# Kernel optimization log

Measured on AMD Instinct MI355X. Metric: run time of the kernel, lower is better.

## Reference

```python
import jax, jax.numpy as jnp
import numpy as np

B, S, D, H, DFF = 4, 1024, 1024, 16, 4096
DK = D // H
EPS = 1e-6


def setup_inputs() -> dict:
    key = jax.random.key(0)
    ks = jax.random.split(key, 16)
    sd = 0.02
    inp = {
        "x_v": jax.random.normal(ks[0], (B, S, D), jnp.float32),
        "x_k": jax.random.normal(ks[1], (B, S, D), jnp.float32),
        "x_q": jax.random.normal(ks[2], (B, S, D), jnp.float32),
        "mask": jnp.zeros((B, 1, S), jnp.float32),
        # per-head projections stacked: [H, D, DK]
        "wq": jax.random.normal(ks[3], (H, D, DK), jnp.float32) * sd,
        "bq": jnp.zeros((H, DK), jnp.float32),
        "wk": jax.random.normal(ks[4], (H, D, DK), jnp.float32) * sd,
        "bk": jnp.zeros((H, DK), jnp.float32),
        "wv": jax.random.normal(ks[5], (H, D, DK), jnp.float32) * sd,
        "bv": jnp.zeros((H, DK), jnp.float32),
        "w0": jax.random.normal(ks[6], (D, D), jnp.float32) * sd,
        "b0": jnp.zeros((D,), jnp.float32),
        "ln1_g": jnp.ones((D,), jnp.float32),
        "ln1_b": jnp.zeros((D,), jnp.float32),
        "ff1_w": jax.random.normal(ks[7], (D, DFF), jnp.float32) * sd,
        "ff1_b": jnp.zeros((DFF,), jnp.float32),
        "ff2_w": jax.random.normal(ks[8], (DFF, D), jnp.float32) * sd,
        "ff2_b": jnp.zeros((D,), jnp.float32),
        "ln2_g": jnp.ones((D,), jnp.float32),
        "ln2_b": jnp.zeros((D,), jnp.float32),
    }
    return inp


def layer_norm(x, g, b):
    mu = jnp.mean(x, axis=-1, keepdims=True)
    var = jnp.mean(jnp.square(x - mu), axis=-1, keepdims=True)
    return (x - mu) * jax.lax.rsqrt(var + EPS) * g + b


def reference(x_v, x_k, x_q, mask, wq, bq, wk, bk, wv, bv, w0, b0,
              ln1_g, ln1_b, ff1_w, ff1_b, ff2_w, ff2_b, ln2_g, ln2_b):
    # --- Multi-head attention (heads batched instead of Python loop) ---
    q = jnp.einsum('bsd,hdk->bhsk', x_q, wq) + bq[:, None, :]  # [B,H,S,DK]
    k = jnp.einsum('bsd,hdk->bhsk', x_k, wk) + bk[:, None, :]
    v = jnp.einsum('bsd,hdk->bhsk', x_v, wv) + bv[:, None, :]
    scores = jnp.einsum('bhqk,bhsk->bhqs', q, k) / jnp.sqrt(jnp.float32(DK))
    scores = scores + mask[:, None, :, :] * (-1e9)  # mask broadcast over heads
    attn_w = jax.nn.softmax(scores, axis=-1)        # [B,H,S,S]
    attn = jnp.einsum('bhqs,bhsk->bhqk', attn_w, v)  # [B,H,S,DK]
    concat = attn.transpose(0, 2, 1, 3).reshape(B, S, D)
    mha_out = concat @ w0 + b0
    # --- Residual + LayerNorm 1 (dropout is identity at inference) ---
    sub1 = layer_norm(x_q + mha_out, ln1_g, ln1_b)
    # --- Point-wise FFN ---
    ffn = jax.nn.relu(sub1 @ ff1_w + ff1_b) @ ff2_w + ff2_b
    # --- Residual + LayerNorm 2 ---
    out = layer_norm(sub1 + ffn, ln2_g, ln2_b)
    # original returns the attention weights of the LAST head only
    return out, attn_w[:, -1]
```

## Files before the change

### kernel.cpp

```cpp
#include <hip/hip_runtime.h>
#include <hip/hip_bf16.h>
#include <stdint.h>

#define DEV __device__ __forceinline__

typedef uint16_t u16;
typedef __attribute__((ext_vector_type(8))) short s16x8;
typedef __attribute__((ext_vector_type(8))) unsigned short u16x8;
typedef __attribute__((ext_vector_type(4))) unsigned short u16x4;
typedef __attribute__((ext_vector_type(4))) float f32x4;

constexpr int CB = 4;
constexpr int CS = 1024;
constexpr int CD = 1024;
constexpr int CH = 16;
constexpr int CDFF = 4096;
constexpr int KVB = 128;
constexpr int LSTRP = 136;
constexpr float QSCALE = 0.125f * 1.44269504f;
constexpr float MASKC  = -1.44269504e9f;

DEV float b2f(u16 u) { union { uint32_t i; float f; } v; v.i = (uint32_t)u << 16; return v.f; }
DEV u16 f2b(float f) {
  union { float f; uint32_t i; } v; v.f = f;
  uint32_t r = v.i + 0x7fffu + ((v.i >> 16) & 1u);
  return (u16)(r >> 16);
}
DEV float ex2(float x) {
#if __has_builtin(__builtin_amdgcn_exp2f)
  return __builtin_amdgcn_exp2f(x);
#else
  return __expf(x * 0.69314718056f);
#endif
}

using as1v = const __attribute__((address_space(1))) void;
using as3v = __attribute__((address_space(3))) void;
DEV void g2l16(const u16* g, u16* l) {
  __builtin_amdgcn_global_load_lds((as1v*)g, (as3v*)l, 16, 0, 0);
}

__global__ void detect_dtype(const uint32_t* __restrict__ w, uint32_t* __restrict__ flag) {
  if (threadIdx.x == 0 && blockIdx.x == 0) {
    flag[0] = (w[0] == 0x3F800000u) ? 1u : 0u;
    flag[1] = 0u;
  }
}

__global__ __launch_bounds__(256)
void cvt3(const void* __restrict__ s0, const void* __restrict__ s1, const void* __restrict__ s2,
          u16* __restrict__ d0, u16* __restrict__ d1, u16* __restrict__ d2,
          const uint32_t* __restrict__ flag)
{
  const void* s = blockIdx.z == 0 ? s0 : (blockIdx.z == 1 ? s1 : s2);
  u16* d        = blockIdx.z == 0 ? d0 : (blockIdx.z == 1 ? d1 : d2);
  size_t i = ((size_t)blockIdx.x * 256 + threadIdx.x) * 4;
  if (flag[0]) {
    const float* f = (const float*)s;
    u16x4 o;
#pragma unroll
    for (int j = 0; j < 4; j++) o[j] = f2b(f[i + j]);
    *(u16x4*)(d + i) = o;
  } else {
    *(u16x4*)(d + i) = *(const u16x4*)((const u16*)s + i);
  }
}

struct SmallCvt {
  const void* src[11];
  u16* dst[11];
  int n[11];
};
__global__ __launch_bounds__(256)
void cvt_small(SmallCvt sc, const uint32_t* __restrict__ flag)
{
  int idx = blockIdx.x * 256 + threadIdx.x;
#pragma unroll
  for (int a = 0; a < 11; a++) {
    if (idx < sc.n[a]) {
      if (flag[0]) sc.dst[a][idx] = f2b(((const float*)sc.src[a])[idx]);
      else         sc.dst[a][idx] = ((const u16*)sc.src[a])[idx];
      return;
    }
    idx -= sc.n[a];
  }
}

__global__ __launch_bounds__(256)
void transpose64d(const void* __restrict__ in, u16* __restrict__ out,
                  int in_rs, long long in_ys, long long in_zs,
                  int out_rs, long long out_ys, long long out_zs,
                  const uint32_t* __restrict__ flag)
{
  int t = blockIdx.x * 256 + threadIdx.x;
  int k  = t & 63;
  int n8 = t >> 6;
  size_t ib = (size_t)blockIdx.z * in_zs + (size_t)blockIdx.y * in_ys
            + (size_t)n8 * 8 * in_rs + k;
  u16* ob = out + (size_t)blockIdx.z * out_zs + (size_t)blockIdx.y * out_ys
                + (size_t)k * out_rs + (size_t)n8 * 8;
  u16x8 v;
  if (flag[0]) {
    const float* f = (const float*)in;
#pragma unroll
    for (int j = 0; j < 8; j++) v[j] = f2b(f[ib + (size_t)j * in_rs]);
  } else {
    const u16* u = (const u16*)in;
#pragma unroll
    for (int j = 0; j < 8; j++) v[j] = u[ib + (size_t)j * in_rs];
  }
  *(u16x8*)ob = v;
}

struct TBatch {
  const void* in[6];
  u16* out[6];
  int in_rs[6];
  long long in_ys[6];
  int out_rs[6];
  long long out_ys[6];
  int nx[6];
  int cnt[6];
};
__global__ __launch_bounds__(256)
void transpose_batch(TBatch tb, const uint32_t* __restrict__ flag)
{
  int rem = blockIdx.x;
  int e = 0;
  while (e < 5 && rem >= tb.cnt[e]) { rem -= tb.cnt[e]; e++; }
  const int bx = rem % tb.nx[e];
  const int by = rem / tb.nx[e];
  const int in_rs = tb.in_rs[e];
  int t = bx * 256 + threadIdx.x;
  int k  = t & 63;
  int n8 = t >> 6;
  size_t ib = (size_t)by * tb.in_ys[e] + (size_t)n8 * 8 * in_rs + k;
  u16* ob = tb.out[e] + (size_t)by * tb.out_ys[e] + (size_t)k * tb.out_rs[e] + (size_t)n8 * 8;
  u16x8 v;
  if (flag[0]) {
    const float* f = (const float*)tb.in[e];
#pragma unroll
    for (int j = 0; j < 8; j++) v[j] = f2b(f[ib + (size_t)j * in_rs]);
  } else {
    const u16* u = (const u16*)tb.in[e];
#pragma unroll
    for (int j = 0; j < 8; j++) v[j] = u[ib + (size_t)j * in_rs];
  }
  *(u16x8*)ob = v;
}

struct GemmArgs {
  const u16* A[3];
  const u16* Bt[3];
  const u16* bias[3];
  u16* C[3];
  float scales[3];
  int M, N, K;
  int relu;
};

template<int MI, int NI, int WGM, int WGN, int BK>
DEV void gemm_body(const GemmArgs& g)
{
  constexpr int BM = WGM * MI * 16;
  constexpr int BN = WGN * NI * 16;
  constexpr int CPR = BK / 8;
  constexpr int CHA = BM * BK / 2048;
  constexpr int CHB = BN * BK / 2048;

  const int z = blockIdx.z;
  const u16* __restrict__ A    = g.A[z];
  const u16* __restrict__ Bt   = g.Bt[z];
  const u16* __restrict__ bias = g.bias[z];
  u16* __restrict__ C          = g.C[z];
  const float scale = g.scales[z];
  const int N = g.N, K = g.K;

  __shared__ __align__(16) u16 lA[BM * BK];
  __shared__ __align__(16) u16 lB[BN * BK];

  const int tid  = threadIdx.x;
  const int lane = tid & 63;
  const int wave = tid >> 6;
  const int quad = lane >> 4;
  const int l16  = lane & 15;
  const int sw   = l16 & (CPR - 1);
  const int wm = (wave / WGN) * MI * 16;
  const int wn = (wave % WGN) * NI * 16;

  const int flat = blockIdx.y * gridDim.x + blockIdx.x;
  const int nY = gridDim.y;
  const size_t bm = (size_t)(flat % nY) * BM;
  const size_t bn = (size_t)(flat / nY) * BN;

  f32x4 acc[MI][NI];
#pragma unroll
  for (int mi = 0; mi < MI; mi++)
#pragma unroll
    for (int ni = 0; ni < NI; ni++)
#pragma unroll
      for (int r = 0; r < 4; r++) acc[mi][ni][r] = 0.f;

  const u16* Ab = A + bm * K;
  const u16* Bb = Bt + bn * K;

  for (int k0 = 0; k0 < K; k0 += BK) {
#pragma unroll
    for (int i = 0; i < CHA; i++) {
      int c = i * 256 + tid;
      int r = c / CPR, j = c % CPR;
      g2l16(Ab + (size_t)r * K + k0 + ((j ^ (r & (CPR - 1))) * 8), lA + c * 8);
    }
#pragma unroll
    for (int i = 0; i < CHB; i++) {
      int c = i * 256 + tid;
      int r = c / CPR, j = c % CPR;
      g2l16(Bb + (size_t)r * K + k0 + ((j ^ (r & (CPR - 1))) * 8), lB + c * 8);
    }
    __syncthreads();
#pragma unroll
    for (int kk = 0; kk < BK / 32; kk++) {
      s16x8 af[MI], bfr[NI];
#pragma unroll
      for (int mi = 0; mi < MI; mi++)
        af[mi] = *(const s16x8*)(lA + (wm + mi * 16 + l16) * BK + (((kk * 4 + quad) ^ sw) * 8));
#pragma unroll
      for (int ni = 0; ni < NI; ni++)
        bfr[ni] = *(const s16x8*)(lB + (wn + ni * 16 + l16) * BK + (((kk * 4 + quad) ^ sw) * 8));
#pragma unroll
      for (int mi = 0; mi < MI; mi++)
#pragma unroll
        for (int ni = 0; ni < NI; ni++)
          acc[mi][ni] = __builtin_amdgcn_mfma_f32_16x16x32_bf16(af[mi], bfr[ni], acc[mi][ni], 0, 0, 0);
    }
    __syncthreads();
  }

  float bvals[NI];
#pragma unroll
  for (int ni = 0; ni < NI; ni++) bvals[ni] = b2f(bias[bn + wn + ni * 16 + l16]);
#pragma unroll
  for (int mi = 0; mi < MI; mi++) {
#pragma unroll
    for (int r = 0; r < 4; r++) {
      size_t row = bm + wm + mi * 16 + quad * 4 + r;
      u16* crow = C + row * N + bn + wn;
#pragma unroll
      for (int ni = 0; ni < NI; ni++) {
        float v = (acc[mi][ni][r] + bvals[ni]) * scale;
        if (g.relu) v = fmaxf(v, 0.f);
        crow[ni * 16 + l16] = f2b(v);
      }
    }
  }
}

__global__ __launch_bounds__(256, 4) void gemm_qkv (GemmArgs g) { gemm_body<4, 4, 2, 2, 64>(g); }
__global__ __launch_bounds__(256, 4) void gemm_wo  (GemmArgs g) { gemm_body<2, 2, 2, 2, 128>(g); }
__global__ __launch_bounds__(256, 4) void gemm_ffn1(GemmArgs g) { gemm_body<4, 4, 2, 2, 64>(g); }
__global__ __launch_bounds__(256, 4) void gemm_ffn2(GemmArgs g) { gemm_body<2, 2, 2, 2, 128>(g); }

__global__ __launch_bounds__(256, 3)
void flash_attn(const u16* __restrict__ Qb, const u16* __restrict__ Kb,
                const u16* __restrict__ Vt, const u16* __restrict__ mask,
                u16* __restrict__ O, float* __restrict__ ml)
{
  const int b = blockIdx.z;
  const int h = blockIdx.x & 15;
  const int q0 = (blockIdx.x >> 4) * 64;
  const int tid  = threadIdx.x;
  const int lane = tid & 63, wave = tid >> 6;
  const int quad = lane >> 4, l16 = lane & 15;
  const int sw3 = l16 & 7;
  const int sw4 = l16 & 15;

  __shared__ __align__(16) u16 lK[KVB * 64];
  __shared__ __align__(16) u16 lV[64 * KVB];
  __shared__ __align__(16) u16 lP[4][16 * LSTRP];

  s16x8 aq[2];
  {
    const u16* qp = Qb + ((size_t)b * CS + q0 + wave * 16 + l16) * CD + h * 64 + quad * 8;
    aq[0] = *(const s16x8*)qp;
    aq[1] = *(const s16x8*)(qp + 32);
  }

  f32x4 of[4];
  float m_r[4], l_r[4];
#pragma unroll
  for (int nt = 0; nt < 4; nt++)
#pragma unroll
    for (int r = 0; r < 4; r++) of[nt][r] = 0.f;
#pragma unroll
  for (int r = 0; r < 4; r++) { m_r[r] = -3.0e38f; l_r[r] = 0.f; }

  int kRow[4], kJ[4], kOff[4], vRow[4], vJ[4], vOff[4];
#pragma unroll
  for (int i = 0; i < 4; i++) {
    int c = i * 256 + tid;
    kRow[i] = c >> 3;  kJ[i] = c & 7;
    kOff[i] = kRow[i] * 64 + ((kJ[i] ^ (kRow[i] & 7)) * 8);
    vRow[i] = c >> 4;  vJ[i] = c & 15;
    vOff[i] = vRow[i] * KVB + ((vJ[i] ^ (vRow[i] & 15)) * 8);
  }

  const u16* Kbase = Kb + (size_t)b * CS * CD + h * 64;
  const u16* Vbase = Vt + ((size_t)(b * CH + h)) * 64 * CS;
  u16* lPw = lP[wave];

  u16x8 rk[4], rv[4];
#pragma unroll
  for (int i = 0; i < 4; i++) {
    rk[i] = *(const u16x8*)(Kbase + (size_t)kRow[i] * CD + kJ[i] * 8);
    rv[i] = *(const u16x8*)(Vbase + (size_t)vRow[i] * CS + vJ[i] * 8);
  }

  for (int kt = 0; kt < CS / KVB; kt++) {
    __syncthreads();
#pragma unroll
    for (int i = 0; i < 4; i++) {
      *(u16x8*)(lK + kOff[i]) = rk[i];
      *(u16x8*)(lV + vOff[i]) = rv[i];
    }
    __syncthreads();

    if (kt + 1 < CS / KVB) {
#pragma unroll
      for (int i = 0; i < 4; i++) {
        rk[i] = *(const u16x8*)(Kbase + (size_t)((kt + 1) * KVB + kRow[i]) * CD + kJ[i] * 8);
        rv[i] = *(const u16x8*)(Vbase + (size_t)vRow[i] * CS + (kt + 1) * KVB + vJ[i] * 8);
      }
    }

    f32x4 sf[8];
#pragma unroll
    for (int ni = 0; ni < 8; ni++)
#pragma unroll
      for (int r = 0; r < 4; r++) sf[ni][r] = 0.f;
#pragma unroll
    for (int kk = 0; kk < 2; kk++) {
#pragma unroll
      for (int ni = 0; ni < 8; ni++) {
        s16x8 bk = *(const s16x8*)(lK + (ni * 16 + l16) * 64 + (((kk * 4 + quad) ^ sw3) * 8));
        sf[ni] = __builtin_amdgcn_mfma_f32_16x16x32_bf16(aq[kk], bk, sf[ni], 0, 0, 0);
      }
    }
#pragma unroll
    for (int ni = 0; ni < 8; ni++) {
      float mv = b2f(mask[(size_t)b * CS + kt * KVB + ni * 16 + l16]) * MASKC;
#pragma unroll
      for (int r = 0; r < 4; r++) sf[ni][r] += mv;
    }
    float mx[4];
#pragma unroll
    for (int r = 0; r < 4; r++) {
      float a = fmaxf(fmaxf(sf[0][r], sf[1][r]), fmaxf(sf[2][r], sf[3][r]));
      float c = fmaxf(fmaxf(sf[4][r], sf[5][r]), fmaxf(sf[6][r], sf[7][r]));
      mx[r] = fmaxf(a, c);
    }
#pragma unroll
    for (int off = 1; off < 16; off <<= 1)
#pragma unroll
      for (int r = 0; r < 4; r++) mx[r] = fmaxf(mx[r], __shfl_xor(mx[r], off, 16));
    bool ng = (mx[0] <= m_r[0] + 8.f) && (mx[1] <= m_r[1] + 8.f) &&
              (mx[2] <= m_r[2] + 8.f) && (mx[3] <= m_r[3] + 8.f);
    if (!__all(ng)) {
#pragma unroll
      for (int r = 0; r < 4; r++) {
        float mn = fmaxf(m_r[r], mx[r]);
        float al = ex2(m_r[r] - mn);
        m_r[r] = mn;
        l_r[r] *= al;
#pragma unroll
        for (int nt = 0; nt < 4; nt++) of[nt][r] *= al;
      }
    }
    float ps[4] = {0.f, 0.f, 0.f, 0.f};
#pragma unroll
    for (int ni = 0; ni < 8; ni++)
#pragma unroll
      for (int r = 0; r < 4; r++) {
        float p = ex2(sf[ni][r] - m_r[r]);
        sf[ni][r] = p;
        ps[r] += p;
      }
#pragma unroll
    for (int off = 1; off < 16; off <<= 1)
#pragma unroll
      for (int r = 0; r < 4; r++) ps[r] += __shfl_xor(ps[r], off, 16);
#pragma unroll
    for (int r = 0; r < 4; r++) l_r[r] += ps[r];
#pragma unroll
    for (int ni = 0; ni < 8; ni++)
#pragma unroll
      for (int r = 0; r < 4; r++)
        lPw[(quad * 4 + r) * LSTRP + ni * 16 + l16] = f2b(sf[ni][r]);
#pragma unroll
    for (int kk = 0; kk < 4; kk++) {
      s16x8 ap = *(const s16x8*)(lPw + l16 * LSTRP + kk * 32 + quad * 8);
#pragma unroll
      for (int nt = 0; nt < 4; nt++) {
        s16x8 bv = *(const s16x8*)(lV + (nt * 16 + l16) * KVB + (((kk * 4 + quad) ^ sw4) * 8));
        of[nt] = __builtin_amdgcn_mfma_f32_16x16x32_bf16(ap, bv, of[nt], 0, 0, 0);
      }
    }
  }

#pragma unroll
  for (int r = 0; r < 4; r++) {
    float inv = 1.f / l_r[r];
    size_t row = q0 + wave * 16 + quad * 4 + r;
    u16* orow = O + ((size_t)b * CS + row) * CD + h * 64;
#pragma unroll
    for (int nt = 0; nt < 4; nt++) orow[nt * 16 + l16] = f2b(of[nt][r] * inv);
    if (h == CH - 1 && l16 == 0) {
      ml[(size_t)b * CS + row] = m_r[r];
      ml[(size_t)CB * CS + (size_t)b * CS + row] = l_r[r];
    }
  }
}

__global__ __launch_bounds__(256)
void attn_probs(const u16* __restrict__ Qb, const u16* __restrict__ Kb,
                const u16* __restrict__ mask, const float* __restrict__ ml,
                void* __restrict__ outbuf, const uint32_t* __restrict__ flag)
{
  const int b = blockIdx.z;
  const int h = CH - 1;
  const int q0 = blockIdx.x * 64;
  const int tid  = threadIdx.x;
  const int lane = tid & 63, wave = tid >> 6;
  const int quad = lane >> 4, l16 = lane & 15;
  const int sw3 = l16 & 7;
  const size_t OUT1 = (size_t)CB * CS * CD;
  const bool f32out = flag[0] != 0;

  __shared__ __align__(16) u16 lK[KVB * 64];

  s16x8 aq[2];
  {
    const u16* qp = Qb + ((size_t)b * CS + q0 + wave * 16 + l16) * CD + h * 64 + quad * 8;
    aq[0] = *(const s16x8*)qp;
    aq[1] = *(const s16x8*)(qp + 32);
  }
  float mr[4], lr[4];
#pragma unroll
  for (int r = 0; r < 4; r++) {
    size_t row = q0 + wave * 16 + quad * 4 + r;
    mr[r] = ml[(size_t)b * CS + row];
    lr[r] = 1.f / ml[(size_t)CB * CS + (size_t)b * CS + row];
  }
  int kRow[4], kJ[4], kOff[4];
#pragma unroll
  for (int i = 0; i < 4; i++) {
    int c = i * 256 + tid;
    kRow[i] = c >> 3;  kJ[i] = c & 7;
    kOff[i] = kRow[i] * 64 + ((kJ[i] ^ (kRow[i] & 7)) * 8);
  }
  const u16* Kbase = Kb + (size_t)b * CS * CD + h * 64;

  u16x8 rk[4];
#pragma unroll
  for (int i = 0; i < 4; i++)
    rk[i] = *(const u16x8*)(Kbase + (size_t)kRow[i] * CD + kJ[i] * 8);

  for (int kt = 0; kt < CS / KVB; kt++) {
    __syncthreads();
#pragma unroll
    for (int i = 0; i < 4; i++)
      *(u16x8*)(lK + kOff[i]) = rk[i];
    __syncthreads();
    if (kt + 1 < CS / KVB) {
#pragma unroll
      for (int i = 0; i < 4; i++)
        rk[i] = *(const u16x8*)(Kbase + (size_t)((kt + 1) * KVB + kRow[i]) * CD + kJ[i] * 8);
    }
    f32x4 sf[8];
#pragma unroll
    for (int ni = 0; ni < 8; ni++)
#pragma unroll
      for (int r = 0; r < 4; r++) sf[ni][r] = 0.f;
#pragma unroll
    for (int kk = 0; kk < 2; kk++) {
#pragma unroll
      for (int ni = 0; ni < 8; ni++) {
        s16x8 bk = *(const s16x8*)(lK + (ni * 16 + l16) * 64 + (((kk * 4 + quad) ^ sw3) * 8));
        sf[ni] = __builtin_amdgcn_mfma_f32_16x16x32_bf16(aq[kk], bk, sf[ni], 0, 0, 0);
      }
    }
#pragma unroll
    for (int ni = 0; ni < 8; ni++) {
      float mv = b2f(mask[(size_t)b * CS + kt * KVB + ni * 16 + l16]) * MASKC;
#pragma unroll
      for (int r = 0; r < 4; r++) {
        float p = ex2(sf[ni][r] + mv - mr[r]) * lr[r];
        size_t row = q0 + wave * 16 + quad * 4 + r;
        size_t idx = OUT1 + ((size_t)b * CS + row) * CS + kt * KVB + ni * 16 + l16;
        if (f32out) ((float*)outbuf)[idx] = p;
        else        ((u16*)outbuf)[idx] = f2b(p);
      }
    }
  }
}

__global__ __launch_bounds__(256)
void resid_ln(const u16* __restrict__ x, const u16* __restrict__ y,
              const u16* __restrict__ g, const u16* __restrict__ bb,
              void* __restrict__ out, const uint32_t* __restrict__ flag,
              int to_out)
{
  const int row = blockIdx.x;
  const int tid = threadIdx.x;
  __shared__ float rs[4], rs2[4];
  const u16* xr = x + (size_t)row * CD;
  const u16* yr = y + (size_t)row * CD;
  const int base = tid * 4;
  const bool f32out = to_out && (flag[0] != 0);
  const u16x4 xv = *(const u16x4*)(xr + base);
  const u16x4 yv = *(const u16x4*)(yr + base);
  float v[4];
  float s = 0.f, s2 = 0.f;
#pragma unroll
  for (int i = 0; i < 4; i++) {
    float a = b2f(xv[i]) + b2f(yv[i]);
    v[i] = a; s += a; s2 += a * a;
  }
#pragma unroll
  for (int off = 32; off > 0; off >>= 1) {
    s += __shfl_down(s, off, 64);
    s2 += __shfl_down(s2, off, 64);
  }
  if ((tid & 63) == 0) { rs[tid >> 6] = s; rs2[tid >> 6] = s2; }
  __syncthreads();
  float st = rs[0] + rs[1] + rs[2] + rs[3];
  float s2t = rs2[0] + rs2[1] + rs2[2] + rs2[3];
  float mu = st * (1.f / CD);
  float var = s2t * (1.f / CD) - mu * mu;
  float rstd = rsqrtf(var + 1e-6f);
  const u16x4 gv = *(const u16x4*)(g + base);
  const u16x4 bv = *(const u16x4*)(bb + base);
  float o[4];
#pragma unroll
  for (int i = 0; i < 4; i++)
    o[i] = (v[i] - mu) * rstd * b2f(gv[i]) + b2f(bv[i]);
  if (f32out) {
    f32x4 o4 = {o[0], o[1], o[2], o[3]};
    *(f32x4*)((float*)out + (size_t)row * CD + base) = o4;
  } else {
    u16x4 o4;
#pragma unroll
    for (int i = 0; i < 4; i++) o4[i] = f2b(o[i]);
    *(u16x4*)((u16*)out + (size_t)row * CD + base) = o4;
  }
}

extern "C" void kernel_launch(void* const* d_in, const int* in_sizes, int n_in,
                              void* d_out, int out_size, void* d_ws, size_t ws_size,
                              hipStream_t stream) {
  const void* x_v   = d_in[0];
  const void* x_k   = d_in[1];
  const void* x_q   = d_in[2];
  const void* maskI = d_in[3];
  const void* wq    = d_in[4];
  const void* bq    = d_in[5];
  const void* wk    = d_in[6];
  const void* bk    = d_in[7];
  const void* wv    = d_in[8];
  const void* bv    = d_in[9];
  const void* w0    = d_in[10];
  const void* b0    = d_in[11];
  const void* ln1_g = d_in[12];
  const void* ln1_b = d_in[13];
  const void* ff1_w = d_in[14];
  const void* ff1_b = d_in[15];
  const void* ff2_w = d_in[16];
  const void* ff2_b = d_in[17];
  const void* ln2_g = d_in[18];
  const void* ln2_b = d_in[19];

  u16* ws = (u16*)d_ws;
  size_t off = 0;
  auto alloc = [&](size_t n) { u16* p = ws + off; off += n; return p; };
  const size_t M1 = 1024 * 1024;
  u16* wqT   = alloc(M1);
  u16* wkT   = alloc(M1);
  u16* wvT   = alloc(M1);
  u16* w0T   = alloc(M1);
  u16* ff1T  = alloc(4 * M1);
  u16* ff2T  = alloc(4 * M1);
  u16* Qb    = alloc(4 * M1);
  u16* Kbuf  = alloc(4 * M1);
  u16* Vbuf  = alloc(4 * M1);
  u16* VtB   = alloc(4 * M1);
  u16* Ob    = alloc(4 * M1);
  u16* mha   = alloc(4 * M1);
  u16* sub1  = alloc(4 * M1);
  u16* ffmid = alloc(16 * M1);
  u16* cxq   = alloc(4 * M1);
  u16* cxk   = alloc(4 * M1);
  u16* cxv   = alloc(4 * M1);
  u16* cmask = alloc(4096);
  u16* cbq   = alloc(1024);
  u16* cbk   = alloc(1024);
  u16* cbv   = alloc(1024);
  u16* cb0   = alloc(1024);
  u16* cf1b  = alloc(4096);
  u16* cf2b  = alloc(1024);
  u16* cl1g  = alloc(1024);
  u16* cl1b  = alloc(1024);
  u16* cl2g  = alloc(1024);
  u16* cl2b  = alloc(1024);
  float* ml  = (float*)alloc(16384);
  uint32_t* flag = (uint32_t*)alloc(64);
  if (ws_size < off * sizeof(u16)) return;

  dim3 blk(256);

  detect_dtype<<<dim3(1), dim3(64), 0, stream>>>((const uint32_t*)ln1_g, flag);
  const uint32_t* fIn = flag;
  const uint32_t* fBf = flag + 1;

  cvt3<<<dim3(4096, 1, 3), blk, 0, stream>>>(x_q, x_k, x_v, cxq, cxk, cxv, fIn);
  {
    SmallCvt sc{};
    const void* s[11] = {maskI, bq, bk, bv, b0, ff1_b, ff2_b, ln1_g, ln1_b, ln2_g, ln2_b};
    u16* d[11] = {cmask, cbq, cbk, cbv, cb0, cf1b, cf2b, cl1g, cl1b, cl2g, cl2b};
    int n[11] = {4096, 1024, 1024, 1024, 1024, 4096, 1024, 1024, 1024, 1024, 1024};
    for (int i = 0; i < 11; i++) { sc.src[i] = s[i]; sc.dst[i] = d[i]; sc.n[i] = n[i]; }
    cvt_small<<<dim3(68), blk, 0, stream>>>(sc, fIn);
  }

  {
    TBatch tb{};
    const void* tin[6] = {wq, wk, wv, w0, ff1_w, ff2_w};
    u16* tout[6]       = {wqT, wkT, wvT, w0T, ff1T, ff2T};
    int irs[6]         = {64, 64, 64, CD, CDFF, CD};
    long long iys[6]   = {(long long)CD * 64, (long long)CD * 64, (long long)CD * 64, 64, 64, 64};
    int ors[6]         = {CD, CD, CD, CD, CD, CDFF};
    long long oys[6]   = {64LL * CD, 64LL * CD, 64LL * CD, 64LL * CD, 64LL * CD, 64LL * CDFF};
    int nx[6]          = {32, 32, 32, 32, 32, 128};
    int cnt[6]         = {512, 512, 512, 512, 2048, 2048};
    for (int i = 0; i < 6; i++) {
      tb.in[i] = tin[i]; tb.out[i] = tout[i];
      tb.in_rs[i] = irs[i]; tb.in_ys[i] = iys[i];
      tb.out_rs[i] = ors[i]; tb.out_ys[i] = oys[i];
      tb.nx[i] = nx[i]; tb.cnt[i] = cnt[i];
    }
    transpose_batch<<<dim3(6144), blk, 0, stream>>>(tb, fIn);
  }

  {
    GemmArgs ga{};
    ga.A[0] = cxq;  ga.A[1] = cxk;  ga.A[2] = cxv;
    ga.Bt[0] = wqT; ga.Bt[1] = wkT; ga.Bt[2] = wvT;
    ga.bias[0] = cbq; ga.bias[1] = cbk; ga.bias[2] = cbv;
    ga.C[0] = Qb; ga.C[1] = Kbuf; ga.C[2] = Vbuf;
    ga.scales[0] = QSCALE; ga.scales[1] = 1.f; ga.scales[2] = 1.f;
    ga.M = CB * CS; ga.N = CD; ga.K = CD; ga.relu = 0;
    gemm_qkv<<<dim3(8, 32, 3), blk, 0, stream>>>(ga);
  }

  transpose64d<<<dim3(32, 16, 4), blk, 0, stream>>>(Vbuf, VtB, CD, 64, (long long)CS * CD,
                                                    CS, 64LL * CS, (long long)CH * 64 * CS, fBf);

  flash_attn<<<dim3(256, 1, CB), blk, 0, stream>>>(Qb, Kbuf, VtB, cmask, Ob, ml);

  attn_probs<<<dim3(CS / 64, 1, CB), blk, 0, stream>>>(Qb, Kbuf, cmask, ml, d_out, fIn);

  {
    GemmArgs ga{};
    ga.A[0] = Ob; ga.Bt[0] = w0T; ga.bias[0] = cb0; ga.C[0] = mha;
    ga.scales[0] = 1.f;
    ga.M = CB * CS; ga.N = CD; ga.K = CD; ga.relu = 0;
    gemm_wo<<<dim3(16, 64, 1), blk, 0, stream>>>(ga);
  }

  resid_ln<<<dim3(CB * CS), blk, 0, stream>>>(cxq, mha, cl1g, cl1b, sub1, fIn, 0);

  {
    GemmArgs ga{};
    ga.A[0] = sub1; ga.Bt[0] = ff1T; ga.bias[0] = cf1b; ga.C[0] = ffmid;
    ga.scales[0] = 1.f;
    ga.M = CB * CS; ga.N = CDFF; ga.K = CD; ga.relu = 1;
    gemm_ffn1<<<dim3(32, 32, 1), blk, 0, stream>>>(ga);
  }

  {
    GemmArgs ga{};
    ga.A[0] = ffmid; ga.Bt[0] = ff2T; ga.bias[0] = cf2b; ga.C[0] = mha;
    ga.scales[0] = 1.f;
    ga.M = CB * CS; ga.N = CD; ga.K = CDFF; ga.relu = 0;
    gemm_ffn2<<<dim3(16, 64, 1), blk, 0, stream>>>(ga);
  }

  resid_ln<<<dim3(CB * CS), blk, 0, stream>>>(sub1, mha, cl2g, cl2b, d_out, fIn, 1);
}
```

Measured before the change: 415.3 us.

## Use intra-block split-K GEMM for W0 and FFN2 projections

Adds a 64x64-tile GEMM variant where each of the four waves computes a different 32-wide K slice of every BK=128 chunk over the full tile. Partial accumulators are then reduced through LDS in two stages before wave 0 applies bias, scale and relu and writes the output. It is applied to the narrow-N W0 and FFN2 GEMMs and is meant to give each wave more MFMA work per LDS fragment load. In exchange it adds LDS reduction traffic and extra barriers, leaves three waves idle during the epilogue, and lowers the occupancy hint to 3. The generic body's chunk count is also made to depend on thread count instead of a fixed 256.

```diff
diff --git a/kernel.cpp b/kernel.cpp
--- a/kernel.cpp
+++ b/kernel.cpp
@@ -164,9 +164,10 @@
 {
   constexpr int BM = WGM * MI * 16;
   constexpr int BN = WGN * NI * 16;
+  constexpr int NT = WGM * WGN * 64;
   constexpr int CPR = BK / 8;
-  constexpr int CHA = BM * BK / 2048;
-  constexpr int CHB = BN * BK / 2048;
+  constexpr int CHA = BM * BK / (NT * 8);
+  constexpr int CHB = BN * BK / (NT * 8);
 
   const int z = blockIdx.z;
   const u16* __restrict__ A    = g.A[z];
@@ -207,13 +208,13 @@
   for (int k0 = 0; k0 < K; k0 += BK) {
 #pragma unroll
     for (int i = 0; i < CHA; i++) {
-      int c = i * 256 + tid;
+      int c = i * NT + tid;
       int r = c / CPR, j = c % CPR;
       g2l16(Ab + (size_t)r * K + k0 + ((j ^ (r & (CPR - 1))) * 8), lA + c * 8);
     }
 #pragma unroll
     for (int i = 0; i < CHB; i++) {
-      int c = i * 256 + tid;
+      int c = i * NT + tid;
       int r = c / CPR, j = c % CPR;
       g2l16(Bb + (size_t)r * K + k0 + ((j ^ (r & (CPR - 1))) * 8), lB + c * 8);
     }
@@ -255,10 +256,140 @@
   }
 }
 
+template<int BK>
+DEV void gemm_body_sk(const GemmArgs& g)
+{
+  constexpr int BM = 64, BN = 64;
+  constexpr int CPR = BK / 8;
+  constexpr int CHA = BM * BK / 2048;
+  constexpr int CHB = BN * BK / 2048;
+
+  const int z = blockIdx.z;
+  const u16* __restrict__ A    = g.A[z];
+  const u16* __restrict__ Bt   = g.Bt[z];
+  const u16* __restrict__ bias = g.bias[z];
+  u16* __restrict__ C          = g.C[z];
+  const float scale = g.scales[z];
+  const int N = g.N, K = g.K;
+
+  __shared__ __align__(16) u16 lA[BM * BK];
+  __shared__ __align__(16) u16 lB[BN * BK];
+
+  const int tid  = threadIdx.x;
+  const int lane = tid & 63;
+  const int wave = tid >> 6;
+  const int quad = lane >> 4;
+  const int l16  = lane & 15;
+  const int sw   = l16 & (CPR - 1);
+
+  const int flat = blockIdx.y * gridDim.x + blockIdx.x;
+  const int nY = gridDim.y;
+  const size_t bm = (size_t)(flat % nY) * BM;
+  const size_t bn = (size_t)(flat / nY) * BN;
+
+  f32x4 acc[4][4];
+#pragma unroll
+  for (int mi = 0; mi < 4; mi++)
+#pragma unroll
+    for (int ni = 0; ni < 4; ni++)
+#pragma unroll
+      for (int r = 0; r < 4; r++) acc[mi][ni][r] = 0.f;
+
+  const u16* Ab = A + bm * K;
+  const u16* Bb = Bt + bn * K;
+
+  for (int k0 = 0; k0 < K; k0 += BK) {
+#pragma unroll
+    for (int i = 0; i < CHA; i++) {
+      int c = i * 256 + tid;
+      int r = c / CPR, j = c % CPR;
+      g2l16(Ab + (size_t)r * K + k0 + ((j ^ (r & (CPR - 1))) * 8), lA + c * 8);
+    }
+#pragma unroll
+    for (int i = 0; i < CHB; i++) {
+      int c = i * 256 + tid;
+      int r = c / CPR, j = c % CPR;
+      g2l16(Bb + (size_t)r * K + k0 + ((j ^ (r & (CPR - 1))) * 8), lB + c * 8);
+    }
+    __syncthreads();
+    {
+      s16x8 af[4], bfr[4];
+      const int ck = ((wave * 4 + quad) ^ sw) * 8;
+#pragma unroll
+      for (int mi = 0; mi < 4; mi++)
+        af[mi] = *(const s16x8*)(lA + (mi * 16 + l16) * BK + ck);
+#pragma unroll
+      for (int ni = 0; ni < 4; ni++)
+        bfr[ni] = *(const s16x8*)(lB + (ni * 16 + l16) * BK + ck);
+#pragma unroll
+      for (int mi = 0; mi < 4; mi++)
+#pragma unroll
+        for (int ni = 0; ni < 4; ni++)
+          acc[mi][ni] = __builtin_amdgcn_mfma_f32_16x16x32_bf16(af[mi], bfr[ni], acc[mi][ni], 0, 0, 0);
+    }
+    __syncthreads();
+  }
+
+  float* red0 = (float*)lA;
+  float* red1 = (float*)lB;
+  if (wave == 1 || wave == 3) {
+    float* dst = (wave == 1) ? red0 : red1;
+#pragma unroll
+    for (int mi = 0; mi < 4; mi++)
+#pragma unroll
+      for (int r = 0; r < 4; r++)
+#pragma unroll
+        for (int ni = 0; ni < 4; ni++)
+          dst[(mi * 16 + quad * 4 + r) * 64 + ni * 16 + l16] = acc[mi][ni][r];
+  }
+  __syncthreads();
+  if (wave == 0 || wave == 2) {
+    float* src = (wave == 0) ? red0 : red1;
+#pragma unroll
+    for (int mi = 0; mi < 4; mi++)
+#pragma unroll
+      for (int r = 0; r < 4; r++)
+#pragma unroll
+        for (int ni = 0; ni < 4; ni++)
+          acc[mi][ni][r] += src[(mi * 16 + quad * 4 + r) * 64 + ni * 16 + l16];
+  }
+  __syncthreads();
+  if (wave == 2) {
+#pragma unroll
+    for (int mi = 0; mi < 4; mi++)
+#pragma unroll
+      for (int r = 0; r < 4; r++)
+#pragma unroll
+        for (int ni = 0; ni < 4; ni++)
+          red0[(mi * 16 + quad * 4 + r) * 64 + ni * 16 + l16] = acc[mi][ni][r];
+  }
+  __syncthreads();
+  if (wave == 0) {
+    float bvals[4];
+#pragma unroll
+    for (int ni = 0; ni < 4; ni++) bvals[ni] = b2f(bias[bn + ni * 16 + l16]);
+#pragma unroll
+    for (int mi = 0; mi < 4; mi++) {
+#pragma unroll
+      for (int r = 0; r < 4; r++) {
+        size_t row = bm + mi * 16 + quad * 4 + r;
+        u16* crow = C + row * N + bn;
+#pragma unroll
+        for (int ni = 0; ni < 4; ni++) {
+          float v = acc[mi][ni][r] + red0[(mi * 16 + quad * 4 + r) * 64 + ni * 16 + l16];
+          v = (v + bvals[ni]) * scale;
+          if (g.relu) v = fmaxf(v, 0.f);
+          crow[ni * 16 + l16] = f2b(v);
+        }
+      }
+    }
+  }
+}
+
 __global__ __launch_bounds__(256, 4) void gemm_qkv (GemmArgs g) { gemm_body<4, 4, 2, 2, 64>(g); }
-__global__ __launch_bounds__(256, 4) void gemm_wo  (GemmArgs g) { gemm_body<2, 2, 2, 2, 128>(g); }
+__global__ __launch_bounds__(256, 3) void gemm_wo  (GemmArgs g) { gemm_body_sk<128>(g); }
 __global__ __launch_bounds__(256, 4) void gemm_ffn1(GemmArgs g) { gemm_body<4, 4, 2, 2, 64>(g); }
-__global__ __launch_bounds__(256, 4) void gemm_ffn2(GemmArgs g) { gemm_body<2, 2, 2, 2, 128>(g); }
+__global__ __launch_bounds__(256, 3) void gemm_ffn2(GemmArgs g) { gemm_body_sk<128>(g); }
 
 __global__ __launch_bounds__(256, 3)
 void flash_attn(const u16* __restrict__ Qb, const u16* __restrict__ Kb,
```

After: 409.1 us. Within noise of the previous version (-1.5%).
